# Performance work log

Hardware: AMD Instinct MI355X
Metric: run time of the kernel (lower is better)

Reference implementation:

```python
import jax, jax.numpy as jnp
import numpy as np

HEAD = 16
EPS = 1.1920929e-07  # torch.finfo(float32).eps, used by nn.RMSNorm when eps=None


def _rms(x, g):
    return x * jax.lax.rsqrt(jnp.mean(x * x, axis=-1, keepdims=True) + EPS) * g


def _heads(t):
    b, L, dm = t.shape
    return t.reshape(b, L, HEAD, dm // HEAD).transpose(0, 2, 1, 3)  # b h L d


def setup_inputs() -> dict:
    key = jax.random.key(0)
    ks = jax.random.split(key, 8)
    b, L, dims = 1, 1024, 1024
    s = dims ** -0.5
    x = jax.random.normal(ks[0], (b, L, dims), jnp.float32)
    pt = jax.random.normal(ks[1], (b, L, dims), jnp.float32)
    # additive causal mask (finite large-negative to stay grad-safe)
    mask = jnp.triu(jnp.full((L, L), -1e9, jnp.float32), k=1)
    return {
        "x": x, "pt": pt, "mask": mask,
        "gq": jnp.ones((dims,), jnp.float32),
        "Wq": jax.random.normal(ks[2], (dims, dims), jnp.float32) * s,
        "bq": jnp.zeros((dims,), jnp.float32),
        "gkv": jnp.ones((dims,), jnp.float32),
        "Wkv": jax.random.normal(ks[3], (dims, 2 * dims), jnp.float32) * s,
        "bkv": jnp.zeros((2 * dims,), jnp.float32),
        "gc": jnp.ones((dims,), jnp.float32),
        "Wc": jax.random.normal(ks[4], (dims, dims), jnp.float32) * s,
        "bc": jnp.zeros((dims,), jnp.float32),
        "Wout": jax.random.normal(ks[5], (dims, dims), jnp.float32) * s,
        "bout": jnp.zeros((dims,), jnp.float32),
        "context_window": 16,
    }


def reference(x, pt, mask, gq, Wq, bq, gkv, Wkv, bkv, gc, Wc, bc, Wout, bout, context_window):
    b, L, dims = x.shape
    d = dims // HEAD
    q = _heads(_rms(x, gq) @ Wq + bq)                      # b h L d
    kv = (_rms(x, gkv) @ Wkv + bkv).reshape(b, L, 2, HEAD, d)
    k = kv[:, :, 0].transpose(0, 2, 1, 3)                  # b h L d
    v = kv[:, :, 1].transpose(0, 2, 1, 3)
    c = _heads(_rms(pt, gc) @ Wc + bc)                     # b h L d

    # triplet_scores[i,j] = sum_{t=max(0,min(i,j)-w)}^{min(L,max(i,j)+w)-1} q_i . (k_j * c_t)
    # Vectorize with prefix sums over c: window sum = P[end] - P[start],
    # where end depends only on max(i,j) and start only on min(i,j).
    P = jnp.concatenate([jnp.zeros((b, HEAD, 1, d), x.dtype), jnp.cumsum(c, axis=2)], axis=2)  # b h L+1 d
    idx = jnp.arange(L)
    S = jnp.clip(idx - context_window, 0, L)   # start for min-index
    E = jnp.clip(idx + context_window, 0, L)   # end for max-index
    PE = jnp.take(P, E, axis=2)                # b h L d
    PS = jnp.take(P, S, axis=2)

    U = jnp.einsum('bhid,bhjd->bhij', q, k * PE)        # end from j (i<=j branch)
    V = jnp.einsum('bhid,bhjd->bhij', q * PS, k)        # start from i (i<=j branch)
    U2 = jnp.einsum('bhid,bhjd->bhij', q * PE, k)       # end from i (i>j branch)
    V2 = jnp.einsum('bhid,bhjd->bhij', q, k * PS)       # start from j (i>j branch)
    lower = idx[:, None] <= idx[None, :]
    triplet = jnp.where(lower, U - V, U2 - V2)          # b h L L

    scale = d ** -0.5
    qk = jnp.einsum('bhid,bhjd->bhij', q, k) * scale + triplet + mask[:L, :L]
    attn = jax.nn.softmax(qk, axis=-1)
    wv = jnp.einsum('bhij,bhjd->bhid', attn, v)
    out = wv.transpose(0, 2, 1, 3).reshape(b, L, dims) @ Wout + bout  # dropout p=0.01 is identity at eval
    return out
```

## Files before the change

### kernel.cpp

```cpp
#include <hip/hip_runtime.h>

#define LQ 1024
#define DM 1024


typedef __attribute__((ext_vector_type(8))) short bf16x8;
typedef __attribute__((ext_vector_type(4))) float f32x4;

#define MFMA(a, b, c) __builtin_amdgcn_mfma_f32_16x16x32_bf16((a), (b), (c), 0, 0, 0)

__device__ __forceinline__ unsigned short f2bf(float x) {
    unsigned int u = __float_as_uint(x);
    return (unsigned short)((u + 0x7FFFu + ((u >> 16) & 1u)) >> 16);
}
__device__ __forceinline__ float bf2f(unsigned short h) {
    return __uint_as_float(((unsigned int)h) << 16);
}
__device__ __forceinline__ void gload16(const void* gp, void* lp) {
    __builtin_amdgcn_global_load_lds(
        (const __attribute__((address_space(1))) void*)gp,
        (__attribute__((address_space(3))) void*)lp, 16, 0, 0);
}
__device__ __forceinline__ void store_split4(unsigned short* ph, unsigned short* pl,
                                             float4 v) {
    unsigned short h0 = f2bf(v.x), h1 = f2bf(v.y), h2 = f2bf(v.z), h3 = f2bf(v.w);
    uint2 a;
    a.x = (unsigned)h0 | ((unsigned)h1 << 16);
    a.y = (unsigned)h2 | ((unsigned)h3 << 16);
    *(uint2*)ph = a;
    unsigned short l0 = f2bf(v.x - bf2f(h0)), l1 = f2bf(v.y - bf2f(h1));
    unsigned short l2 = f2bf(v.z - bf2f(h2)), l3 = f2bf(v.w - bf2f(h3));
    uint2 b;
    b.x = (unsigned)l0 | ((unsigned)l1 << 16);
    b.y = (unsigned)l2 | ((unsigned)l3 << 16);
    *(uint2*)pl = b;
}

__global__ __launch_bounds__(256) void rms_kernel(
    const float* __restrict__ x, const float* __restrict__ pt,
    const float* __restrict__ gq, const float* __restrict__ gkv,
    const float* __restrict__ gc,
    unsigned short* __restrict__ xqn_h, unsigned short* __restrict__ xqn_l,
    unsigned short* __restrict__ xkvn_h, unsigned short* __restrict__ xkvn_l,
    unsigned short* __restrict__ ptn_h, unsigned short* __restrict__ ptn_l)
{
    const int row = blockIdx.x;
    const int t = threadIdx.x;
    const bool isx = row < LQ;
    const float* src = isx ? (x + (size_t)row * DM)
                           : (pt + (size_t)(row - LQ) * DM);
    float4 v = ((const float4*)src)[t];
    float ss = v.x*v.x + v.y*v.y + v.z*v.z + v.w*v.w;
    #pragma unroll
    for (int o = 32; o > 0; o >>= 1) ss += __shfl_down(ss, o);
    __shared__ float red[4];
    if ((t & 63) == 0) red[t >> 6] = ss;
    __syncthreads();
    const float r = rsqrtf((red[0] + red[1] + red[2] + red[3]) * (1.0f / DM)
                           + 1.1920929e-07f);
    const size_t base = (size_t)(isx ? row : row - LQ) * DM + t * 4;
    if (isx) {
        float4 g1 = ((const float4*)gq)[t];
        float4 g2 = ((const float4*)gkv)[t];
        float4 y1, y2;
        y1.x = v.x*r*g1.x; y1.y = v.y*r*g1.y; y1.z = v.z*r*g1.z; y1.w = v.w*r*g1.w;
        y2.x = v.x*r*g2.x; y2.y = v.y*r*g2.y; y2.z = v.z*r*g2.z; y2.w = v.w*r*g2.w;
        store_split4(xqn_h + base, xqn_l + base, y1);
        store_split4(xkvn_h + base, xkvn_l + base, y2);
    } else {
        float4 g = ((const float4*)gc)[t];
        float4 y;
        y.x = v.x*r*g.x; y.y = v.y*r*g.y; y.z = v.z*r*g.z; y.w = v.w*r*g.w;
        store_split4(ptn_h + base, ptn_l + base, y);
    }
}

__global__ __launch_bounds__(256) void wsplit_kernel(
    const float* __restrict__ in, unsigned short* __restrict__ oh,
    unsigned short* __restrict__ ol, int K, int N)
{
    __shared__ float T[64 * 65];
    const int t = threadIdx.x;
    const int tx = t & 15, ty = t >> 4;
    const int c0 = blockIdx.x * 64;
    const int r0 = blockIdx.y * 64;
    #pragma unroll
    for (int p = 0; p < 4; ++p) {
        int row = ty + p * 16;
        float4 v = *(const float4*)(in + (size_t)(r0 + row) * N + c0 + tx * 4);
        T[row * 65 + tx * 4 + 0] = v.x;
        T[row * 65 + tx * 4 + 1] = v.y;
        T[row * 65 + tx * 4 + 2] = v.z;
        T[row * 65 + tx * 4 + 3] = v.w;
    }
    __syncthreads();
    #pragma unroll
    for (int p = 0; p < 4; ++p) {
        int n = ty + p * 16;
        float4 w;
        w.x = T[(tx * 4 + 0) * 65 + n];
        w.y = T[(tx * 4 + 1) * 65 + n];
        w.z = T[(tx * 4 + 2) * 65 + n];
        w.w = T[(tx * 4 + 3) * 65 + n];
        size_t o = (size_t)(c0 + n) * K + r0 + tx * 4;
        store_split4(oh + o, ol + o, w);
    }
}

__device__ __forceinline__ void gemm_mfma_128(
    const unsigned short* __restrict__ Ah, const unsigned short* __restrict__ Al,
    const unsigned short* __restrict__ Bh, const unsigned short* __restrict__ Bl,
    const float* __restrict__ bias, float* __restrict__ out, int N, int mt, int nt)
{
    __shared__ unsigned short sA[2][128 * 32];
    __shared__ unsigned short sB[2][128 * 32];
    const int t = threadIdx.x;
    const int lane = t & 63, wid = t >> 6;
    const int wm = wid >> 1, wn = wid & 1;
    const int n16 = lane & 15, quad = lane >> 4;
    f32x4 zero = {0.f, 0.f, 0.f, 0.f};
    f32x4 acc[4][4];
    #pragma unroll
    for (int ms = 0; ms < 4; ++ms)
        #pragma unroll
        for (int ns = 0; ns < 4; ++ns) acc[ms][ns] = zero;

    const int arow = wid * 16 + (lane >> 2);
    const int acol = (lane & 3) * 8;
    for (int kt = 0; kt < 32; ++kt) {
        const int k0 = kt * 32;
        #pragma unroll
        for (int p = 0; p < 2; ++p) {
            const int row = arow + p * 64;
            const size_t ga = (size_t)(mt * 128 + row) * 1024 + k0 + acol;
            const size_t gb = (size_t)(nt * 128 + row) * 1024 + k0 + acol;
            const int lo = p * 2048 + wid * 512;
            gload16(Ah + ga, &sA[0][lo]);
            gload16(Al + ga, &sA[1][lo]);
            gload16(Bh + gb, &sB[0][lo]);
            gload16(Bl + gb, &sB[1][lo]);
        }
        __syncthreads();
        bf16x8 afh[4], afl[4], bfh[4], bfl[4];
        #pragma unroll
        for (int ms = 0; ms < 4; ++ms) {
            int r = wm * 64 + ms * 16 + n16;
            afh[ms] = *(const bf16x8*)&sA[0][r * 32 + quad * 8];
            afl[ms] = *(const bf16x8*)&sA[1][r * 32 + quad * 8];
        }
        #pragma unroll
        for (int ns = 0; ns < 4; ++ns) {
            int r = wn * 64 + ns * 16 + n16;
            bfh[ns] = *(const bf16x8*)&sB[0][r * 32 + quad * 8];
            bfl[ns] = *(const bf16x8*)&sB[1][r * 32 + quad * 8];
        }
        #pragma unroll
        for (int ms = 0; ms < 4; ++ms)
            #pragma unroll
            for (int ns = 0; ns < 4; ++ns) {
                acc[ms][ns] = MFMA(afh[ms], bfh[ns], acc[ms][ns]);
                acc[ms][ns] = MFMA(afh[ms], bfl[ns], acc[ms][ns]);
                acc[ms][ns] = MFMA(afl[ms], bfh[ns], acc[ms][ns]);
            }
        __syncthreads();
    }
    #pragma unroll
    for (int ns = 0; ns < 4; ++ns) {
        const int col = nt * 128 + wn * 64 + ns * 16 + n16;
        const float bv = bias[col];
        #pragma unroll
        for (int ms = 0; ms < 4; ++ms) {
            const int row0 = mt * 128 + wm * 64 + ms * 16 + quad * 4;
            #pragma unroll
            for (int reg = 0; reg < 4; ++reg)
                out[(size_t)(row0 + reg) * N + col] = acc[ms][ns][reg] + bv;
        }
    }
}

__global__ __launch_bounds__(256) void proj_kernel(
    const unsigned short* __restrict__ xqn_h, const unsigned short* __restrict__ xqn_l,
    const unsigned short* __restrict__ xkvn_h, const unsigned short* __restrict__ xkvn_l,
    const unsigned short* __restrict__ ptn_h, const unsigned short* __restrict__ ptn_l,
    const unsigned short* __restrict__ WqT_h, const unsigned short* __restrict__ WqT_l,
    const unsigned short* __restrict__ WkvT_h, const unsigned short* __restrict__ WkvT_l,
    const unsigned short* __restrict__ WcT_h, const unsigned short* __restrict__ WcT_l,
    const float* __restrict__ bq, const float* __restrict__ bkv,
    const float* __restrict__ bc,
    float* __restrict__ Qb, float* __restrict__ KVb, float* __restrict__ Cb)
{
    const int bid = blockIdx.x;
    if (bid < 64) {
        gemm_mfma_128(xqn_h, xqn_l, WqT_h, WqT_l, bq, Qb, 1024, bid >> 3, bid & 7);
    } else if (bid < 192) {
        int b2 = bid - 64;
        gemm_mfma_128(xkvn_h, xkvn_l, WkvT_h, WkvT_l, bkv, KVb, 2048, b2 >> 4, b2 & 15);
    } else {
        int b2 = bid - 192;
        gemm_mfma_128(ptn_h, ptn_l, WcT_h, WcT_l, bc, Cb, 1024, b2 >> 3, b2 & 7);
    }
}

__global__ __launch_bounds__(128) void outgemm_kernel(
    const unsigned short* __restrict__ Ah, const unsigned short* __restrict__ Al,
    const unsigned short* __restrict__ Bh, const unsigned short* __restrict__ Bl,
    const float* __restrict__ bias, float* __restrict__ out)
{
    __shared__ unsigned short sA[2][64 * 32];
    __shared__ unsigned short sB[2][64 * 32];
    const int t = threadIdx.x;
    const int lane = t & 63, w = t >> 6;
    const int n16 = lane & 15, quad = lane >> 4;
    const int mt = blockIdx.y, nt = blockIdx.x;
    f32x4 zero = {0.f, 0.f, 0.f, 0.f};
    f32x4 acc[2][4];
    #pragma unroll
    for (int ms = 0; ms < 2; ++ms)
        #pragma unroll
        for (int ns = 0; ns < 4; ++ns) acc[ms][ns] = zero;

    const int arow = w * 16 + (lane >> 2);
    const int acol = (lane & 3) * 8;
    for (int kt = 0; kt < 32; ++kt) {
        const int k0 = kt * 32;
        #pragma unroll
        for (int p = 0; p < 2; ++p) {
            const int row = arow + p * 32;
            const size_t ga = (size_t)(mt * 64 + row) * 1024 + k0 + acol;
            const size_t gb = (size_t)(nt * 64 + row) * 1024 + k0 + acol;
            const int lo = p * 1024 + w * 512;
            gload16(Ah + ga, &sA[0][lo]);
            gload16(Al + ga, &sA[1][lo]);
            gload16(Bh + gb, &sB[0][lo]);
            gload16(Bl + gb, &sB[1][lo]);
        }
        __syncthreads();
        bf16x8 afh[2], afl[2], bfh[4], bfl[4];
        #pragma unroll
        for (int ms = 0; ms < 2; ++ms) {
            int r = w * 32 + ms * 16 + n16;
            afh[ms] = *(const bf16x8*)&sA[0][r * 32 + quad * 8];
            afl[ms] = *(const bf16x8*)&sA[1][r * 32 + quad * 8];
        }
        #pragma unroll
        for (int ns = 0; ns < 4; ++ns) {
            int r = ns * 16 + n16;
            bfh[ns] = *(const bf16x8*)&sB[0][r * 32 + quad * 8];
            bfl[ns] = *(const bf16x8*)&sB[1][r * 32 + quad * 8];
        }
        #pragma unroll
        for (int ms = 0; ms < 2; ++ms)
            #pragma unroll
            for (int ns = 0; ns < 4; ++ns) {
                acc[ms][ns] = MFMA(afh[ms], bfh[ns], acc[ms][ns]);
                acc[ms][ns] = MFMA(afh[ms], bfl[ns], acc[ms][ns]);
                acc[ms][ns] = MFMA(afl[ms], bfh[ns], acc[ms][ns]);
            }
        __syncthreads();
    }
    #pragma unroll
    for (int ns = 0; ns < 4; ++ns) {
        const int col = nt * 64 + ns * 16 + n16;
        const float bv = bias[col];
        #pragma unroll
        for (int ms = 0; ms < 2; ++ms) {
            const int row0 = mt * 64 + w * 32 + ms * 16 + quad * 4;
            #pragma unroll
            for (int reg = 0; reg < 4; ++reg)
                out[(size_t)(row0 + reg) * 1024 + col] = acc[ms][ns][reg] + bv;
        }
    }
}

__global__ __launch_bounds__(256) void csum_kernel(const float* __restrict__ Cb,
                                                   float* __restrict__ csum)
{
    const int cid = blockIdx.x >> 2;
    const int col = ((blockIdx.x & 3) << 8) + threadIdx.x;
    const float* p = Cb + (size_t)cid * 32 * 1024 + col;
    float s = 0.f;
    #pragma unroll 8
    for (int r = 0; r < 32; ++r) s += p[(size_t)r * 1024];
    csum[cid * 1024 + col] = s;
}

__global__ __launch_bounds__(256) void scanp_kernel(const float* __restrict__ Cb,
                                                    const float* __restrict__ csum,
                                                    float* __restrict__ Pb)
{
    const int cid = blockIdx.x >> 2;
    const int col = ((blockIdx.x & 3) << 8) + threadIdx.x;
    float run = 0.f;
    for (int c = 0; c < cid; ++c) run += csum[c * 1024 + col];
    const float* p = Cb + (size_t)cid * 32 * 1024 + col;
    float* q = Pb + (size_t)cid * 32 * 1024 + col;
    for (int r = 0; r < 32; ++r) {
        q[(size_t)r * 1024] = run;
        run += p[(size_t)r * 1024];
    }
    if (cid == 31) Pb[(size_t)1024 * 1024 + col] = run;
}

__global__ __launch_bounds__(256) void ab_kernel(
    const float* __restrict__ Qb, const float* __restrict__ KVb,
    const float* __restrict__ Pb, const int* __restrict__ cwp,
    unsigned short* __restrict__ Aah, unsigned short* __restrict__ Aal,
    unsigned short* __restrict__ Bah, unsigned short* __restrict__ Bal)
{
    const int gid = blockIdx.x * 256 + threadIdx.x;
    const int i = gid >> 10;
    const int col = gid & 1023;
    const int h = col >> 6, dd = col & 63;
    const int cw = *cwp;
    const int E = min(i + cw, LQ);
    const int S = max(i - cw, 0);
    const float pe = Pb[(size_t)E * 1024 + col];
    const float ps = Pb[(size_t)S * 1024 + col];
    const float q = Qb[gid];
    const float k = KVb[(size_t)i * 2048 + col];
    const float scale = 0.125f;
    const size_t base = ((size_t)(h * 1024 + i)) * 128;
    float a0 = q, a1 = q * pe;
    float b0 = k * (scale - ps), b1 = k;
    unsigned short hv;
    hv = f2bf(a0); Aah[base + dd] = hv;      Aal[base + dd] = f2bf(a0 - bf2f(hv));
    hv = f2bf(a1); Aah[base + 64 + dd] = hv; Aal[base + 64 + dd] = f2bf(a1 - bf2f(hv));
    hv = f2bf(b0); Bah[base + dd] = hv;      Bal[base + dd] = f2bf(b0 - bf2f(hv));
    hv = f2bf(b1); Bah[base + 64 + dd] = hv; Bal[base + 64 + dd] = f2bf(b1 - bf2f(hv));
}

__global__ __launch_bounds__(256) void vprep_kernel(const float* __restrict__ KVb,
                                                    unsigned short* __restrict__ VT)
{
    __shared__ float T[64 * 65];
    const int h = blockIdx.y, j0 = blockIdx.x * 64;
    const int t = threadIdx.x;
    const int tx = t & 15, ty = t >> 4;
    #pragma unroll
    for (int p = 0; p < 4; ++p) {
        int j = ty + p * 16;
        float4 v = *(const float4*)(KVb + (size_t)(j0 + j) * 2048 + 1024 + h * 64 + tx * 4);
        T[j * 65 + tx * 4 + 0] = v.x;
        T[j * 65 + tx * 4 + 1] = v.y;
        T[j * 65 + tx * 4 + 2] = v.z;
        T[j * 65 + tx * 4 + 3] = v.w;
    }
    __syncthreads();
    #pragma unroll
    for (int p = 0; p < 4; ++p) {
        int d = ty + p * 16;
        unsigned short e0 = f2bf(T[(tx * 4 + 0) * 65 + d]);
        unsigned short e1 = f2bf(T[(tx * 4 + 1) * 65 + d]);
        unsigned short e2 = f2bf(T[(tx * 4 + 2) * 65 + d]);
        unsigned short e3 = f2bf(T[(tx * 4 + 3) * 65 + d]);
        uint2 pk;
        pk.x = (unsigned)e0 | ((unsigned)e1 << 16);
        pk.y = (unsigned)e2 | ((unsigned)e3 << 16);
        *(uint2*)(VT + (size_t)(h * 64 + d) * 1024 + j0 + tx * 4) = pk;
    }
}

__global__ __launch_bounds__(128) void attn_kernel(
    const unsigned short* __restrict__ Aah, const unsigned short* __restrict__ Aal,
    const unsigned short* __restrict__ Bah, const unsigned short* __restrict__ Bal,
    const unsigned short* __restrict__ VT,
    unsigned short* __restrict__ wvh, unsigned short* __restrict__ wvl)
{
    __shared__ unsigned short sA[2][32 * 136];
    __shared__ unsigned short sB[2][64 * 136];
    unsigned short* Ps = sB[0];
    unsigned short* Vs = sB[0] + 32 * 136;

    const int t = threadIdx.x;
    const int lane = t & 63, w = t >> 6;
    const int n16 = lane & 15, quad = lane >> 4;
    const int b = blockIdx.x;
    const int g = b >> 8, rr = b & 255;
    const int h = rr & 15;
    const int it = g ? (rr >> 4) : (31 - (rr >> 4));
    const int i0 = it * 32;
    const int njt = (it >> 1) + 1;

    {
        const int r = t >> 2;
        const int cb = (t & 3) * 32;
        const unsigned short* gh = Aah + ((size_t)(h * 1024 + i0 + r)) * 128 + cb;
        const unsigned short* gl = Aal + ((size_t)(h * 1024 + i0 + r)) * 128 + cb;
        #pragma unroll
        for (int u = 0; u < 4; ++u) {
            *(uint4*)&sA[0][r * 136 + cb + u * 8] = *(const uint4*)(gh + u * 8);
            *(uint4*)&sA[1][r * 136 + cb + u * 8] = *(const uint4*)(gl + u * 8);
        }
    }

    f32x4 zero = {0.f, 0.f, 0.f, 0.f};
    f32x4 oacc[4];
    #pragma unroll
    for (int dt = 0; dt < 4; ++dt) oacc[dt] = zero;
    float mrow[4], lrow[4];
    #pragma unroll
    for (int reg = 0; reg < 4; ++reg) { mrow[reg] = -1e30f; lrow[reg] = 0.f; }

    for (int jt64 = 0; jt64 < njt; ++jt64) {
        const int j0 = jt64 * 64;
        __syncthreads();
        {
            const int r = t >> 1;
            const int cb = (t & 1) * 64;
            const unsigned short* gh = Bah + ((size_t)(h * 1024 + j0 + r)) * 128 + cb;
            const unsigned short* gl = Bal + ((size_t)(h * 1024 + j0 + r)) * 128 + cb;
            #pragma unroll
            for (int u = 0; u < 8; ++u) {
                *(uint4*)&sB[0][r * 136 + cb + u * 8] = *(const uint4*)(gh + u * 8);
                *(uint4*)&sB[1][r * 136 + cb + u * 8] = *(const uint4*)(gl + u * 8);
            }
        }
        __syncthreads();

        bf16x8 afh[4], afl[4];
        #pragma unroll
        for (int kc = 0; kc < 4; ++kc) {
            int r = w * 16 + n16;
            afh[kc] = *(const bf16x8*)&sA[0][r * 136 + kc * 32 + quad * 8];
            afl[kc] = *(const bf16x8*)&sA[1][r * 136 + kc * 32 + quad * 8];
        }
        f32x4 s[4];
        #pragma unroll
        for (int jt = 0; jt < 4; ++jt) s[jt] = zero;
        #pragma unroll
        for (int jt = 0; jt < 4; ++jt) {
            #pragma unroll
            for (int kc = 0; kc < 4; ++kc) {
                int r = jt * 16 + n16;
                bf16x8 bh = *(const bf16x8*)&sB[0][r * 136 + kc * 32 + quad * 8];
                bf16x8 bl = *(const bf16x8*)&sB[1][r * 136 + kc * 32 + quad * 8];
                s[jt] = MFMA(afh[kc], bh, s[jt]);
                s[jt] = MFMA(afh[kc], bl, s[jt]);
                s[jt] = MFMA(afl[kc], bh, s[jt]);
            }
        }
        if (jt64 == njt - 1) {
            const int ibase = i0 + w * 16 + quad * 4;
            #pragma unroll
            for (int jt = 0; jt < 4; ++jt) {
                const int j = j0 + jt * 16 + n16;
                #pragma unroll
                for (int reg = 0; reg < 4; ++reg)
                    if (j > ibase + reg) s[jt][reg] = -1e30f;
            }
        }

        float alpha[4];
        #pragma unroll
        for (int reg = 0; reg < 4; ++reg) {
            float mt_ = fmaxf(fmaxf(s[0][reg], s[1][reg]), fmaxf(s[2][reg], s[3][reg]));
            mt_ = fmaxf(mt_, __shfl_xor(mt_, 1));
            mt_ = fmaxf(mt_, __shfl_xor(mt_, 2));
            mt_ = fmaxf(mt_, __shfl_xor(mt_, 4));
            mt_ = fmaxf(mt_, __shfl_xor(mt_, 8));
            const float mn = fmaxf(mrow[reg], mt_);
            alpha[reg] = __expf(mrow[reg] - mn);
            mrow[reg] = mn;
            float rs = 0.f;
            #pragma unroll
            for (int jt = 0; jt < 4; ++jt) {
                float p = __expf(s[jt][reg] - mn);
                s[jt][reg] = p;
                rs += p;
            }
            rs += __shfl_xor(rs, 1); rs += __shfl_xor(rs, 2);
            rs += __shfl_xor(rs, 4); rs += __shfl_xor(rs, 8);
            lrow[reg] = lrow[reg] * alpha[reg] + rs;
        }

        __syncthreads();
        #pragma unroll
        for (int jt = 0; jt < 4; ++jt)
            #pragma unroll
            for (int reg = 0; reg < 4; ++reg)
                Ps[(w * 16 + quad * 4 + reg) * 136 + jt * 16 + n16] = f2bf(s[jt][reg]);
        {
            const int r = t >> 1;
            const int cb = (t & 1) * 32;
            const unsigned short* gv = VT + ((size_t)(h * 64 + r)) * 1024 + j0 + cb;
            #pragma unroll
            for (int u = 0; u < 4; ++u)
                *(uint4*)&Vs[r * 136 + cb + u * 8] = *(const uint4*)(gv + u * 8);
        }
        __syncthreads();

        #pragma unroll
        for (int dt = 0; dt < 4; ++dt)
            #pragma unroll
            for (int reg = 0; reg < 4; ++reg)
                oacc[dt][reg] *= alpha[reg];
        bf16x8 pf[2];
        #pragma unroll
        for (int kc = 0; kc < 2; ++kc)
            pf[kc] = *(const bf16x8*)&Ps[(w * 16 + n16) * 136 + kc * 32 + quad * 8];
        #pragma unroll
        for (int dt = 0; dt < 4; ++dt)
            #pragma unroll
            for (int kc = 0; kc < 2; ++kc) {
                bf16x8 vf = *(const bf16x8*)&Vs[(dt * 16 + n16) * 136 + kc * 32 + quad * 8];
                oacc[dt] = MFMA(pf[kc], vf, oacc[dt]);
            }
    }

    float inv[4];
    #pragma unroll
    for (int reg = 0; reg < 4; ++reg) inv[reg] = 1.0f / lrow[reg];
    #pragma unroll
    for (int dt = 0; dt < 4; ++dt) {
        #pragma unroll
        for (int reg = 0; reg < 4; ++reg) {
            const float v = oacc[dt][reg] * inv[reg];
            const size_t idx = (size_t)(i0 + w * 16 + quad * 4 + reg) * 1024
                             + h * 64 + dt * 16 + n16;
            const unsigned short hv = f2bf(v);
            wvh[idx] = hv;
            wvl[idx] = f2bf(v - bf2f(hv));
        }
    }
}

extern "C" void kernel_launch(void* const* d_in, const int* in_sizes, int n_in,
                              void* d_out, int out_size, void* d_ws, size_t ws_size,
                              hipStream_t stream) {
    (void)in_sizes; (void)n_in; (void)out_size; (void)ws_size;
    const float* x    = (const float*)d_in[0];
    const float* pt   = (const float*)d_in[1];
    const float* gq   = (const float*)d_in[3];
    const float* Wq   = (const float*)d_in[4];
    const float* bq   = (const float*)d_in[5];
    const float* gkv  = (const float*)d_in[6];
    const float* Wkv  = (const float*)d_in[7];
    const float* bkv  = (const float*)d_in[8];
    const float* gc   = (const float*)d_in[9];
    const float* Wc   = (const float*)d_in[10];
    const float* bc   = (const float*)d_in[11];
    const float* Wout = (const float*)d_in[12];
    const float* bout = (const float*)d_in[13];
    const int*   cw   = (const int*)d_in[14];
    float* out = (float*)d_out;

    char* W = (char*)d_ws;
    const size_t MB = 1u << 20;
    #define US(off) ((unsigned short*)(W + (off)))
    #define FP(off) ((float*)(W + (off)))
    unsigned short* xqn_h  = US(0 * MB);
    unsigned short* xqn_l  = US(2 * MB);
    unsigned short* xkvn_h = US(4 * MB);
    unsigned short* xkvn_l = US(6 * MB);
    unsigned short* ptn_h  = US(8 * MB);
    unsigned short* ptn_l  = US(10 * MB);
    unsigned short* WqT_h  = US(12 * MB);
    unsigned short* WqT_l  = US(14 * MB);
    unsigned short* WkvT_h = US(16 * MB);
    unsigned short* WkvT_l = US(20 * MB);
    unsigned short* WcT_h  = US(24 * MB);
    unsigned short* WcT_l  = US(26 * MB);
    unsigned short* WoutT_h = US(28 * MB);
    unsigned short* WoutT_l = US(30 * MB);
    float* Qb   = FP(32 * MB);
    float* KVb  = FP(36 * MB);
    float* Cb   = FP(44 * MB);
    float* Pb   = FP(48 * MB);
    float* csum = FP(53 * MB);
    unsigned short* Aah = US(0 * MB);
    unsigned short* Aal = US(4 * MB);
    unsigned short* Bah = US(8 * MB);
    unsigned short* Bal = US(12 * MB);
    unsigned short* VTb = US(16 * MB);
    unsigned short* wv_h = US(18 * MB);
    unsigned short* wv_l = US(20 * MB);
    #undef US
    #undef FP

    hipLaunchKernelGGL(rms_kernel, dim3(2048), dim3(256), 0, stream,
                       x, pt, gq, gkv, gc, xqn_h, xqn_l, xkvn_h, xkvn_l, ptn_h, ptn_l);
    hipLaunchKernelGGL(wsplit_kernel, dim3(16, 16), dim3(256), 0, stream,
                       Wq, WqT_h, WqT_l, 1024, 1024);
    hipLaunchKernelGGL(wsplit_kernel, dim3(32, 16), dim3(256), 0, stream,
                       Wkv, WkvT_h, WkvT_l, 1024, 2048);
    hipLaunchKernelGGL(wsplit_kernel, dim3(16, 16), dim3(256), 0, stream,
                       Wc, WcT_h, WcT_l, 1024, 1024);
    hipLaunchKernelGGL(wsplit_kernel, dim3(16, 16), dim3(256), 0, stream,
                       Wout, WoutT_h, WoutT_l, 1024, 1024);
    hipLaunchKernelGGL(proj_kernel, dim3(256), dim3(256), 0, stream,
                       xqn_h, xqn_l, xkvn_h, xkvn_l, ptn_h, ptn_l,
                       WqT_h, WqT_l, WkvT_h, WkvT_l, WcT_h, WcT_l,
                       bq, bkv, bc, Qb, KVb, Cb);
    hipLaunchKernelGGL(csum_kernel, dim3(128), dim3(256), 0, stream, Cb, csum);
    hipLaunchKernelGGL(scanp_kernel, dim3(128), dim3(256), 0, stream, Cb, csum, Pb);
    hipLaunchKernelGGL(ab_kernel, dim3(4096), dim3(256), 0, stream,
                       Qb, KVb, Pb, cw, Aah, Aal, Bah, Bal);
    hipLaunchKernelGGL(vprep_kernel, dim3(16, 16), dim3(256), 0, stream, KVb, VTb);
    hipLaunchKernelGGL(attn_kernel, dim3(512), dim3(128), 0, stream,
                       Aah, Aal, Bah, Bal, VTb, wv_h, wv_l);
    hipLaunchKernelGGL(outgemm_kernel, dim3(16, 16), dim3(128), 0, stream,
                       wv_h, wv_l, WoutT_h, WoutT_l, bout, out);
}
```

Measured before the change: 246.2 us.

## Fuse prep kernels, split attention over key halves, merge partials in out-GEMM

Merges the RMS-norm and four weight-split kernels into one launch, and the ab and vprep kernels into another, cutting launch count. The projection GEMM tile now uses 512 threads with a smaller per-wave N sub-tile. Attention becomes split-K: each wave handles 16 query rows for one head and half of the key range, and writes unnormalised partial outputs plus running max and sum. The output GEMM then combines the two partials with log-sum-exp weights while loading its A tile. The aim is more parallelism and better load balance in attention, in exchange for extra fp32 partial traffic and merge work.

New measurement: 276.4 us. 1.12x slower.

```diff
diff --git a/kernel.cpp b/kernel.cpp
--- a/kernel.cpp
+++ b/kernel.cpp
@@ -36,15 +36,14 @@
     *(uint2*)pl = b;
 }
 
-__global__ __launch_bounds__(256) void rms_kernel(
-    const float* __restrict__ x, const float* __restrict__ pt,
+__device__ __forceinline__ void rms_body(
+    int row, const float* __restrict__ x, const float* __restrict__ pt,
     const float* __restrict__ gq, const float* __restrict__ gkv,
     const float* __restrict__ gc,
-    unsigned short* __restrict__ xqn_h, unsigned short* __restrict__ xqn_l,
-    unsigned short* __restrict__ xkvn_h, unsigned short* __restrict__ xkvn_l,
-    unsigned short* __restrict__ ptn_h, unsigned short* __restrict__ ptn_l)
-{
-    const int row = blockIdx.x;
+    unsigned short* xqn_h, unsigned short* xqn_l,
+    unsigned short* xkvn_h, unsigned short* xkvn_l,
+    unsigned short* ptn_h, unsigned short* ptn_l)
+{
     const int t = threadIdx.x;
     const bool isx = row < LQ;
     const float* src = isx ? (x + (size_t)row * DM)
@@ -75,15 +74,14 @@
     }
 }
 
-__global__ __launch_bounds__(256) void wsplit_kernel(
-    const float* __restrict__ in, unsigned short* __restrict__ oh,
-    unsigned short* __restrict__ ol, int K, int N)
+__device__ __forceinline__ void wsplit_body(
+    const float* __restrict__ in, unsigned short* oh, unsigned short* ol,
+    int K, int N, int bx, int by)
 {
     __shared__ float T[64 * 65];
     const int t = threadIdx.x;
     const int tx = t & 15, ty = t >> 4;
-    const int c0 = blockIdx.x * 64;
-    const int r0 = blockIdx.y * 64;
+    const int c0 = bx * 64, r0 = by * 64;
     #pragma unroll
     for (int p = 0; p < 4; ++p) {
         int row = ty + p * 16;
@@ -107,66 +105,89 @@
     }
 }
 
-__device__ __forceinline__ void gemm_mfma_128(
+__global__ __launch_bounds__(256) void prep_kernel(
+    const float* __restrict__ x, const float* __restrict__ pt,
+    const float* __restrict__ gq, const float* __restrict__ gkv,
+    const float* __restrict__ gc,
+    const float* __restrict__ Wq, const float* __restrict__ Wkv,
+    const float* __restrict__ Wc, const float* __restrict__ Wout,
+    unsigned short* xqn_h, unsigned short* xqn_l,
+    unsigned short* xkvn_h, unsigned short* xkvn_l,
+    unsigned short* ptn_h, unsigned short* ptn_l,
+    unsigned short* WqT_h, unsigned short* WqT_l,
+    unsigned short* WkvT_h, unsigned short* WkvT_l,
+    unsigned short* WcT_h, unsigned short* WcT_l,
+    unsigned short* WoT_h, unsigned short* WoT_l)
+{
+    const int b = blockIdx.x;
+    if (b < 2048) {
+        rms_body(b, x, pt, gq, gkv, gc, xqn_h, xqn_l, xkvn_h, xkvn_l, ptn_h, ptn_l);
+    } else if (b < 2304) {
+        int s = b - 2048; wsplit_body(Wq, WqT_h, WqT_l, 1024, 1024, s & 15, s >> 4);
+    } else if (b < 2816) {
+        int s = b - 2304; wsplit_body(Wkv, WkvT_h, WkvT_l, 1024, 2048, s & 31, s >> 5);
+    } else if (b < 3072) {
+        int s = b - 2816; wsplit_body(Wc, WcT_h, WcT_l, 1024, 1024, s & 15, s >> 4);
+    } else {
+        int s = b - 3072; wsplit_body(Wout, WoT_h, WoT_l, 1024, 1024, s & 15, s >> 4);
+    }
+}
+
+__device__ __forceinline__ void gemm3p(
     const unsigned short* __restrict__ Ah, const unsigned short* __restrict__ Al,
     const unsigned short* __restrict__ Bh, const unsigned short* __restrict__ Bl,
     const float* __restrict__ bias, float* __restrict__ out, int N, int mt, int nt)
 {
-    __shared__ unsigned short sA[2][128 * 32];
-    __shared__ unsigned short sB[2][128 * 32];
+    __shared__ unsigned short sAh[128 * 32], sAl[128 * 32];
+    __shared__ unsigned short sBh[128 * 32], sBl[128 * 32];
     const int t = threadIdx.x;
-    const int lane = t & 63, wid = t >> 6;
-    const int wm = wid >> 1, wn = wid & 1;
+    const int lane = t & 63, w = t >> 6;
+    const int wm = w >> 2, wn = w & 3;
     const int n16 = lane & 15, quad = lane >> 4;
+    const int srow = lane >> 2, scol = (lane & 3) * 8;
     f32x4 zero = {0.f, 0.f, 0.f, 0.f};
-    f32x4 acc[4][4];
+    f32x4 acc[4][2];
     #pragma unroll
     for (int ms = 0; ms < 4; ++ms)
         #pragma unroll
-        for (int ns = 0; ns < 4; ++ns) acc[ms][ns] = zero;
-
-    const int arow = wid * 16 + (lane >> 2);
-    const int acol = (lane & 3) * 8;
+        for (int ns = 0; ns < 2; ++ns) acc[ms][ns] = zero;
+
     for (int kt = 0; kt < 32; ++kt) {
         const int k0 = kt * 32;
-        #pragma unroll
-        for (int p = 0; p < 2; ++p) {
-            const int row = arow + p * 64;
-            const size_t ga = (size_t)(mt * 128 + row) * 1024 + k0 + acol;
-            const size_t gb = (size_t)(nt * 128 + row) * 1024 + k0 + acol;
-            const int lo = p * 2048 + wid * 512;
-            gload16(Ah + ga, &sA[0][lo]);
-            gload16(Al + ga, &sA[1][lo]);
-            gload16(Bh + gb, &sB[0][lo]);
-            gload16(Bl + gb, &sB[1][lo]);
-        }
+        const size_t ga = (size_t)(mt * 128 + w * 16 + srow) * 1024 + k0 + scol;
+        const size_t gb = (size_t)(nt * 128 + w * 16 + srow) * 1024 + k0 + scol;
+        const int lb = w * 512;
         __syncthreads();
-        bf16x8 afh[4], afl[4], bfh[4], bfl[4];
+        gload16(Ah + ga, sAh + lb);
+        gload16(Al + ga, sAl + lb);
+        gload16(Bh + gb, sBh + lb);
+        gload16(Bl + gb, sBl + lb);
+        __syncthreads();
+        bf16x8 afh[4], afl[4], bfh[2], bfl[2];
         #pragma unroll
         for (int ms = 0; ms < 4; ++ms) {
             int r = wm * 64 + ms * 16 + n16;
-            afh[ms] = *(const bf16x8*)&sA[0][r * 32 + quad * 8];
-            afl[ms] = *(const bf16x8*)&sA[1][r * 32 + quad * 8];
-        }
-        #pragma unroll
-        for (int ns = 0; ns < 4; ++ns) {
-            int r = wn * 64 + ns * 16 + n16;
-            bfh[ns] = *(const bf16x8*)&sB[0][r * 32 + quad * 8];
-            bfl[ns] = *(const bf16x8*)&sB[1][r * 32 + quad * 8];
+            afh[ms] = *(const bf16x8*)&sAh[r * 32 + quad * 8];
+            afl[ms] = *(const bf16x8*)&sAl[r * 32 + quad * 8];
+        }
+        #pragma unroll
+        for (int ns = 0; ns < 2; ++ns) {
+            int r = wn * 32 + ns * 16 + n16;
+            bfh[ns] = *(const bf16x8*)&sBh[r * 32 + quad * 8];
+            bfl[ns] = *(const bf16x8*)&sBl[r * 32 + quad * 8];
         }
         #pragma unroll
         for (int ms = 0; ms < 4; ++ms)
             #pragma unroll
-            for (int ns = 0; ns < 4; ++ns) {
+            for (int ns = 0; ns < 2; ++ns) {
                 acc[ms][ns] = MFMA(afh[ms], bfh[ns], acc[ms][ns]);
                 acc[ms][ns] = MFMA(afh[ms], bfl[ns], acc[ms][ns]);
                 acc[ms][ns] = MFMA(afl[ms], bfh[ns], acc[ms][ns]);
             }
-        __syncthreads();
-    }
-    #pragma unroll
-    for (int ns = 0; ns < 4; ++ns) {
-        const int col = nt * 128 + wn * 64 + ns * 16 + n16;
+    }
+    #pragma unroll
+    for (int ns = 0; ns < 2; ++ns) {
+        const int col = nt * 128 + wn * 32 + ns * 16 + n16;
         const float bv = bias[col];
         #pragma unroll
         for (int ms = 0; ms < 4; ++ms) {
@@ -178,7 +199,7 @@
     }
 }
 
-__global__ __launch_bounds__(256) void proj_kernel(
+__global__ __launch_bounds__(512) void proj_kernel(
     const unsigned short* __restrict__ xqn_h, const unsigned short* __restrict__ xqn_l,
     const unsigned short* __restrict__ xkvn_h, const unsigned short* __restrict__ xkvn_l,
     const unsigned short* __restrict__ ptn_h, const unsigned short* __restrict__ ptn_l,
@@ -191,84 +212,13 @@
 {
     const int bid = blockIdx.x;
     if (bid < 64) {
-        gemm_mfma_128(xqn_h, xqn_l, WqT_h, WqT_l, bq, Qb, 1024, bid >> 3, bid & 7);
+        gemm3p(xqn_h, xqn_l, WqT_h, WqT_l, bq, Qb, 1024, bid >> 3, bid & 7);
     } else if (bid < 192) {
         int b2 = bid - 64;
-        gemm_mfma_128(xkvn_h, xkvn_l, WkvT_h, WkvT_l, bkv, KVb, 2048, b2 >> 4, b2 & 15);
+        gemm3p(xkvn_h, xkvn_l, WkvT_h, WkvT_l, bkv, KVb, 2048, b2 >> 4, b2 & 15);
     } else {
         int b2 = bid - 192;
-        gemm_mfma_128(ptn_h, ptn_l, WcT_h, WcT_l, bc, Cb, 1024, b2 >> 3, b2 & 7);
-    }
-}
-
-__global__ __launch_bounds__(128) void outgemm_kernel(
-    const unsigned short* __restrict__ Ah, const unsigned short* __restrict__ Al,
-    const unsigned short* __restrict__ Bh, const unsigned short* __restrict__ Bl,
-    const float* __restrict__ bias, float* __restrict__ out)
-{
-    __shared__ unsigned short sA[2][64 * 32];
-    __shared__ unsigned short sB[2][64 * 32];
-    const int t = threadIdx.x;
-    const int lane = t & 63, w = t >> 6;
-    const int n16 = lane & 15, quad = lane >> 4;
-    const int mt = blockIdx.y, nt = blockIdx.x;
-    f32x4 zero = {0.f, 0.f, 0.f, 0.f};
-    f32x4 acc[2][4];
-    #pragma unroll
-    for (int ms = 0; ms < 2; ++ms)
-        #pragma unroll
-        for (int ns = 0; ns < 4; ++ns) acc[ms][ns] = zero;
-
-    const int arow = w * 16 + (lane >> 2);
-    const int acol = (lane & 3) * 8;
-    for (int kt = 0; kt < 32; ++kt) {
-        const int k0 = kt * 32;
-        #pragma unroll
-        for (int p = 0; p < 2; ++p) {
-            const int row = arow + p * 32;
-            const size_t ga = (size_t)(mt * 64 + row) * 1024 + k0 + acol;
-            const size_t gb = (size_t)(nt * 64 + row) * 1024 + k0 + acol;
-            const int lo = p * 1024 + w * 512;
-            gload16(Ah + ga, &sA[0][lo]);
-            gload16(Al + ga, &sA[1][lo]);
-            gload16(Bh + gb, &sB[0][lo]);
-            gload16(Bl + gb, &sB[1][lo]);
-        }
-        __syncthreads();
-        bf16x8 afh[2], afl[2], bfh[4], bfl[4];
-        #pragma unroll
-        for (int ms = 0; ms < 2; ++ms) {
-            int r = w * 32 + ms * 16 + n16;
-            afh[ms] = *(const bf16x8*)&sA[0][r * 32 + quad * 8];
-            afl[ms] = *(const bf16x8*)&sA[1][r * 32 + quad * 8];
-        }
-        #pragma unroll
-        for (int ns = 0; ns < 4; ++ns) {
-            int r = ns * 16 + n16;
-            bfh[ns] = *(const bf16x8*)&sB[0][r * 32 + quad * 8];
-            bfl[ns] = *(const bf16x8*)&sB[1][r * 32 + quad * 8];
-        }
-        #pragma unroll
-        for (int ms = 0; ms < 2; ++ms)
-            #pragma unroll
-            for (int ns = 0; ns < 4; ++ns) {
-                acc[ms][ns] = MFMA(afh[ms], bfh[ns], acc[ms][ns]);
-                acc[ms][ns] = MFMA(afh[ms], bfl[ns], acc[ms][ns]);
-                acc[ms][ns] = MFMA(afl[ms], bfh[ns], acc[ms][ns]);
-            }
-        __syncthreads();
-    }
-    #pragma unroll
-    for (int ns = 0; ns < 4; ++ns) {
-        const int col = nt * 64 + ns * 16 + n16;
-        const float bv = bias[col];
-        #pragma unroll
-        for (int ms = 0; ms < 2; ++ms) {
-            const int row0 = mt * 64 + w * 32 + ms * 16 + quad * 4;
-            #pragma unroll
-            for (int reg = 0; reg < 4; ++reg)
-                out[(size_t)(row0 + reg) * 1024 + col] = acc[ms][ns][reg] + bv;
-        }
+        gemm3p(ptn_h, ptn_l, WcT_h, WcT_l, bc, Cb, 1024, b2 >> 3, b2 & 7);
     }
 }
 
@@ -301,95 +251,92 @@
     if (cid == 31) Pb[(size_t)1024 * 1024 + col] = run;
 }
 
-__global__ __launch_bounds__(256) void ab_kernel(
+__global__ __launch_bounds__(256) void abv_kernel(
     const float* __restrict__ Qb, const float* __restrict__ KVb,
     const float* __restrict__ Pb, const int* __restrict__ cwp,
     unsigned short* __restrict__ Aah, unsigned short* __restrict__ Aal,
-    unsigned short* __restrict__ Bah, unsigned short* __restrict__ Bal)
-{
-    const int gid = blockIdx.x * 256 + threadIdx.x;
-    const int i = gid >> 10;
-    const int col = gid & 1023;
-    const int h = col >> 6, dd = col & 63;
-    const int cw = *cwp;
-    const int E = min(i + cw, LQ);
-    const int S = max(i - cw, 0);
-    const float pe = Pb[(size_t)E * 1024 + col];
-    const float ps = Pb[(size_t)S * 1024 + col];
-    const float q = Qb[gid];
-    const float k = KVb[(size_t)i * 2048 + col];
-    const float scale = 0.125f;
-    const size_t base = ((size_t)(h * 1024 + i)) * 128;
-    float a0 = q, a1 = q * pe;
-    float b0 = k * (scale - ps), b1 = k;
-    unsigned short hv;
-    hv = f2bf(a0); Aah[base + dd] = hv;      Aal[base + dd] = f2bf(a0 - bf2f(hv));
-    hv = f2bf(a1); Aah[base + 64 + dd] = hv; Aal[base + 64 + dd] = f2bf(a1 - bf2f(hv));
-    hv = f2bf(b0); Bah[base + dd] = hv;      Bal[base + dd] = f2bf(b0 - bf2f(hv));
-    hv = f2bf(b1); Bah[base + 64 + dd] = hv; Bal[base + 64 + dd] = f2bf(b1 - bf2f(hv));
-}
-
-__global__ __launch_bounds__(256) void vprep_kernel(const float* __restrict__ KVb,
-                                                    unsigned short* __restrict__ VT)
-{
-    __shared__ float T[64 * 65];
-    const int h = blockIdx.y, j0 = blockIdx.x * 64;
-    const int t = threadIdx.x;
-    const int tx = t & 15, ty = t >> 4;
-    #pragma unroll
-    for (int p = 0; p < 4; ++p) {
-        int j = ty + p * 16;
-        float4 v = *(const float4*)(KVb + (size_t)(j0 + j) * 2048 + 1024 + h * 64 + tx * 4);
-        T[j * 65 + tx * 4 + 0] = v.x;
-        T[j * 65 + tx * 4 + 1] = v.y;
-        T[j * 65 + tx * 4 + 2] = v.z;
-        T[j * 65 + tx * 4 + 3] = v.w;
-    }
-    __syncthreads();
-    #pragma unroll
-    for (int p = 0; p < 4; ++p) {
-        int d = ty + p * 16;
-        unsigned short e0 = f2bf(T[(tx * 4 + 0) * 65 + d]);
-        unsigned short e1 = f2bf(T[(tx * 4 + 1) * 65 + d]);
-        unsigned short e2 = f2bf(T[(tx * 4 + 2) * 65 + d]);
-        unsigned short e3 = f2bf(T[(tx * 4 + 3) * 65 + d]);
-        uint2 pk;
-        pk.x = (unsigned)e0 | ((unsigned)e1 << 16);
-        pk.y = (unsigned)e2 | ((unsigned)e3 << 16);
-        *(uint2*)(VT + (size_t)(h * 64 + d) * 1024 + j0 + tx * 4) = pk;
-    }
-}
-
-__global__ __launch_bounds__(128) void attn_kernel(
+    unsigned short* __restrict__ Bah, unsigned short* __restrict__ Bal,
+    unsigned short* __restrict__ VT)
+{
+    const int b = blockIdx.x;
+    if (b < 4096) {
+        const int gid = b * 256 + threadIdx.x;
+        const int i = gid >> 10;
+        const int col = gid & 1023;
+        const int h = col >> 6, dd = col & 63;
+        const int cw = *cwp;
+        const int E = min(i + cw, LQ);
+        const int S = max(i - cw, 0);
+        const float pe = Pb[(size_t)E * 1024 + col];
+        const float ps = Pb[(size_t)S * 1024 + col];
+        const float q = Qb[gid];
+        const float k = KVb[(size_t)i * 2048 + col];
+        const float scale = 0.125f;
+        const size_t base = ((size_t)(h * 1024 + i)) * 128;
+        float a0 = q, a1 = q * pe;
+        float b0 = k * (scale - ps), b1 = k;
+        unsigned short hv;
+        hv = f2bf(a0); Aah[base + dd] = hv;      Aal[base + dd] = f2bf(a0 - bf2f(hv));
+        hv = f2bf(a1); Aah[base + 64 + dd] = hv; Aal[base + 64 + dd] = f2bf(a1 - bf2f(hv));
+        hv = f2bf(b0); Bah[base + dd] = hv;      Bal[base + dd] = f2bf(b0 - bf2f(hv));
+        hv = f2bf(b1); Bah[base + 64 + dd] = hv; Bal[base + 64 + dd] = f2bf(b1 - bf2f(hv));
+    } else {
+        const int s = b - 4096;
+        const int h = s >> 4, j0 = (s & 15) * 64;
+        __shared__ float T[64 * 65];
+        const int t = threadIdx.x;
+        const int tx = t & 15, ty = t >> 4;
+        #pragma unroll
+        for (int p = 0; p < 4; ++p) {
+            int j = ty + p * 16;
+            float4 v = *(const float4*)(KVb + (size_t)(j0 + j) * 2048 + 1024 + h * 64 + tx * 4);
+            T[j * 65 + tx * 4 + 0] = v.x;
+            T[j * 65 + tx * 4 + 1] = v.y;
+            T[j * 65 + tx * 4 + 2] = v.z;
+            T[j * 65 + tx * 4 + 3] = v.w;
+        }
+        __syncthreads();
+        #pragma unroll
+        for (int p = 0; p < 4; ++p) {
+            int d = ty + p * 16;
+            unsigned short e0 = f2bf(T[(tx * 4 + 0) * 65 + d]);
+            unsigned short e1 = f2bf(T[(tx * 4 + 1) * 65 + d]);
+            unsigned short e2 = f2bf(T[(tx * 4 + 2) * 65 + d]);
+            unsigned short e3 = f2bf(T[(tx * 4 + 3) * 65 + d]);
+            uint2 pk;
+            pk.x = (unsigned)e0 | ((unsigned)e1 << 16);
+            pk.y = (unsigned)e2 | ((unsigned)e3 << 16);
+            *(uint2*)(VT + (size_t)(h * 64 + d) * 1024 + j0 + tx * 4) = pk;
+        }
+    }
+}
+
+__global__ __launch_bounds__(256) void attn_kernel(
     const unsigned short* __restrict__ Aah, const unsigned short* __restrict__ Aal,
     const unsigned short* __restrict__ Bah, const unsigned short* __restrict__ Bal,
     const unsigned short* __restrict__ VT,
-    unsigned short* __restrict__ wvh, unsigned short* __restrict__ wvl)
-{
-    __shared__ unsigned short sA[2][32 * 136];
-    __shared__ unsigned short sB[2][64 * 136];
-    unsigned short* Ps = sB[0];
-    unsigned short* Vs = sB[0] + 32 * 136;
-
+    float* __restrict__ Op, float* __restrict__ Mp, float* __restrict__ Lp)
+{
+    __shared__ unsigned short PsAll[4][16 * 68];
     const int t = threadIdx.x;
-    const int lane = t & 63, w = t >> 6;
+    const int lane = t & 63, wid = t >> 6;
+    unsigned short* Ps = PsAll[wid];
+    const int raw = blockIdx.x * 4 + wid;
+    const int g = raw >> 5;
+    const int it16 = (g & 1) ? (g >> 1) : (63 - (g >> 1));
+    const int sub = raw & 31;
+    const int h = sub >> 1, half = sub & 1;
+    const int i0 = it16 * 16;
+    const int njt = (i0 >> 6) + 1;
     const int n16 = lane & 15, quad = lane >> 4;
-    const int b = blockIdx.x;
-    const int g = b >> 8, rr = b & 255;
-    const int h = rr & 15;
-    const int it = g ? (rr >> 4) : (31 - (rr >> 4));
-    const int i0 = it * 32;
-    const int njt = (it >> 1) + 1;
-
+
+    bf16x8 afh[4], afl[4];
     {
-        const int r = t >> 2;
-        const int cb = (t & 3) * 32;
-        const unsigned short* gh = Aah + ((size_t)(h * 1024 + i0 + r)) * 128 + cb;
-        const unsigned short* gl = Aal + ((size_t)(h * 1024 + i0 + r)) * 128 + cb;
-        #pragma unroll
-        for (int u = 0; u < 4; ++u) {
-            *(uint4*)&sA[0][r * 136 + cb + u * 8] = *(const uint4*)(gh + u * 8);
-            *(uint4*)&sA[1][r * 136 + cb + u * 8] = *(const uint4*)(gl + u * 8);
+        const size_t ar = ((size_t)(h * 1024 + i0 + n16)) * 128 + quad * 8;
+        #pragma unroll
+        for (int kc = 0; kc < 4; ++kc) {
+            afh[kc] = *(const bf16x8*)(Aah + ar + kc * 32);
+            afl[kc] = *(const bf16x8*)(Aal + ar + kc * 32);
         }
     }
 
@@ -401,52 +348,31 @@
     #pragma unroll
     for (int reg = 0; reg < 4; ++reg) { mrow[reg] = -1e30f; lrow[reg] = 0.f; }
 
-    for (int jt64 = 0; jt64 < njt; ++jt64) {
-        const int j0 = jt64 * 64;
-        __syncthreads();
-        {
-            const int r = t >> 1;
-            const int cb = (t & 1) * 64;
-            const unsigned short* gh = Bah + ((size_t)(h * 1024 + j0 + r)) * 128 + cb;
-            const unsigned short* gl = Bal + ((size_t)(h * 1024 + j0 + r)) * 128 + cb;
-            #pragma unroll
-            for (int u = 0; u < 8; ++u) {
-                *(uint4*)&sB[0][r * 136 + cb + u * 8] = *(const uint4*)(gh + u * 8);
-                *(uint4*)&sB[1][r * 136 + cb + u * 8] = *(const uint4*)(gl + u * 8);
+    for (int jt = half; jt < njt; jt += 2) {
+        const int j0 = jt * 64;
+        f32x4 s[4];
+        #pragma unroll
+        for (int jj = 0; jj < 4; ++jj) s[jj] = zero;
+        #pragma unroll
+        for (int jj = 0; jj < 4; ++jj) {
+            const size_t br = ((size_t)(h * 1024 + j0 + jj * 16 + n16)) * 128 + quad * 8;
+            #pragma unroll
+            for (int kc = 0; kc < 4; ++kc) {
+                bf16x8 bh = *(const bf16x8*)(Bah + br + kc * 32);
+                bf16x8 bl = *(const bf16x8*)(Bal + br + kc * 32);
+                s[jj] = MFMA(afh[kc], bh, s[jj]);
+                s[jj] = MFMA(afh[kc], bl, s[jj]);
+                s[jj] = MFMA(afl[kc], bh, s[jj]);
             }
         }
-        __syncthreads();
-
-        bf16x8 afh[4], afl[4];
-        #pragma unroll
-        for (int kc = 0; kc < 4; ++kc) {
-            int r = w * 16 + n16;
-            afh[kc] = *(const bf16x8*)&sA[0][r * 136 + kc * 32 + quad * 8];
-            afl[kc] = *(const bf16x8*)&sA[1][r * 136 + kc * 32 + quad * 8];
-        }
-        f32x4 s[4];
-        #pragma unroll
-        for (int jt = 0; jt < 4; ++jt) s[jt] = zero;
-        #pragma unroll
-        for (int jt = 0; jt < 4; ++jt) {
-            #pragma unroll
-            for (int kc = 0; kc < 4; ++kc) {
-                int r = jt * 16 + n16;
-                bf16x8 bh = *(const bf16x8*)&sB[0][r * 136 + kc * 32 + quad * 8];
-                bf16x8 bl = *(const bf16x8*)&sB[1][r * 136 + kc * 32 + quad * 8];
-                s[jt] = MFMA(afh[kc], bh, s[jt]);
-                s[jt] = MFMA(afh[kc], bl, s[jt]);
-                s[jt] = MFMA(afl[kc], bh, s[jt]);
-            }
-        }
-        if (jt64 == njt - 1) {
-            const int ibase = i0 + w * 16 + quad * 4;
-            #pragma unroll
-            for (int jt = 0; jt < 4; ++jt) {
-                const int j = j0 + jt * 16 + n16;
+        if (jt == njt - 1) {
+            const int ibase = i0 + quad * 4;
+            #pragma unroll
+            for (int jj = 0; jj < 4; ++jj) {
+                const int j = j0 + jj * 16 + n16;
                 #pragma unroll
                 for (int reg = 0; reg < 4; ++reg)
-                    if (j > ibase + reg) s[jt][reg] = -1e30f;
+                    if (j > ibase + reg) s[jj][reg] = -1e30f;
             }
         }
 
@@ -463,9 +389,9 @@
             mrow[reg] = mn;
             float rs = 0.f;
             #pragma unroll
-            for (int jt = 0; jt < 4; ++jt) {
-                float p = __expf(s[jt][reg] - mn);
-                s[jt][reg] = p;
+            for (int jj = 0; jj < 4; ++jj) {
+                float p = __expf(s[jj][reg] - mn);
+                s[jj][reg] = p;
                 rs += p;
             }
             rs += __shfl_xor(rs, 1); rs += __shfl_xor(rs, 2);
@@ -473,53 +399,136 @@
             lrow[reg] = lrow[reg] * alpha[reg] + rs;
         }
 
+        __builtin_amdgcn_s_waitcnt(0xC07F);
+        #pragma unroll
+        for (int jj = 0; jj < 4; ++jj)
+            #pragma unroll
+            for (int reg = 0; reg < 4; ++reg)
+                Ps[(quad * 4 + reg) * 68 + jj * 16 + n16] = f2bf(s[jj][reg]);
+        __builtin_amdgcn_s_waitcnt(0xC07F);
+        bf16x8 pf0 = *(const bf16x8*)&Ps[n16 * 68 + quad * 8];
+        bf16x8 pf1 = *(const bf16x8*)&Ps[n16 * 68 + 32 + quad * 8];
+
+        #pragma unroll
+        for (int dt = 0; dt < 4; ++dt) {
+            #pragma unroll
+            for (int reg = 0; reg < 4; ++reg) oacc[dt][reg] *= alpha[reg];
+            const size_t vr = ((size_t)(h * 64 + dt * 16 + n16)) * 1024 + j0 + quad * 8;
+            bf16x8 vf0 = *(const bf16x8*)(VT + vr);
+            bf16x8 vf1 = *(const bf16x8*)(VT + vr + 32);
+            oacc[dt] = MFMA(pf0, vf0, oacc[dt]);
+            oacc[dt] = MFMA(pf1, vf1, oacc[dt]);
+        }
+    }
+
+    const int tid = (h * 64 + it16) * 2 + half;
+    #pragma unroll
+    for (int dt = 0; dt < 4; ++dt)
+        #pragma unroll
+        for (int reg = 0; reg < 4; ++reg)
+            Op[(size_t)tid * 1024 + (quad * 4 + reg) * 64 + dt * 16 + n16] = oacc[dt][reg];
+    if (n16 == 0) {
+        #pragma unroll
+        for (int reg = 0; reg < 4; ++reg) {
+            Mp[tid * 16 + quad * 4 + reg] = mrow[reg];
+            Lp[tid * 16 + quad * 4 + reg] = lrow[reg];
+        }
+    }
+}
+
+__global__ __launch_bounds__(128) void outgemm_kernel(
+    const float* __restrict__ Op, const float* __restrict__ Mp,
+    const float* __restrict__ Lp,
+    const unsigned short* __restrict__ WoT_h, const unsigned short* __restrict__ WoT_l,
+    const float* __restrict__ bout, float* __restrict__ out)
+{
+    __shared__ float cc[16 * 64 * 2];
+    __shared__ unsigned short sAh[64 * 32], sAl[64 * 32];
+    __shared__ unsigned short sBh[32 * 32], sBl[32 * 32];
+    const int t = threadIdx.x;
+    const int lane = t & 63, w = t >> 6;
+    const int n16 = lane & 15, quad = lane >> 4;
+    const int mt = blockIdx.x >> 5, nt = blockIdx.x & 31;
+
+    for (int p = t; p < 1024; p += 128) {
+        const int hh = p >> 6, row = p & 63;
+        const int i = mt * 64 + row, i16 = i >> 4, r = i & 15;
+        const int t0 = (hh * 64 + i16) * 2;
+        const float m1 = Mp[t0 * 16 + r], m2 = Mp[(t0 + 1) * 16 + r];
+        const float l1 = Lp[t0 * 16 + r], l2 = Lp[(t0 + 1) * 16 + r];
+        const float M = fmaxf(m1, m2);
+        const float e1 = __expf(m1 - M), e2 = __expf(m2 - M);
+        const float Ltot = e1 * l1 + e2 * l2;
+        cc[p * 2 + 0] = e1 / Ltot;
+        cc[p * 2 + 1] = e2 / Ltot;
+    }
+
+    f32x4 zero = {0.f, 0.f, 0.f, 0.f};
+    f32x4 acc[2][2];
+    #pragma unroll
+    for (int ms = 0; ms < 2; ++ms)
+        #pragma unroll
+        for (int ns = 0; ns < 2; ++ns) acc[ms][ns] = zero;
+
+    const int arow = t >> 1, aseg = (t & 1) * 16;
+    for (int kt = 0; kt < 32; ++kt) {
+        const int hh = kt >> 1, dbase = (kt & 1) * 32;
         __syncthreads();
-        #pragma unroll
-        for (int jt = 0; jt < 4; ++jt)
+        {
+            const size_t gb = (size_t)(nt * 32 + w * 16 + (lane >> 2)) * 1024
+                            + kt * 32 + (lane & 3) * 8;
+            gload16(WoT_h + gb, sBh + w * 512);
+            gload16(WoT_l + gb, sBl + w * 512);
+        }
+        {
+            const int i = mt * 64 + arow, i16 = i >> 4, r = i & 15;
+            const float c1 = cc[(hh * 64 + arow) * 2 + 0];
+            const float c2 = cc[(hh * 64 + arow) * 2 + 1];
+            const size_t b0 = ((size_t)((hh * 64 + i16) * 2)) * 1024 + r * 64 + dbase + aseg;
+            #pragma unroll
+            for (int u = 0; u < 4; ++u) {
+                float4 o1 = *(const float4*)(Op + b0 + u * 4);
+                float4 o2 = *(const float4*)(Op + b0 + 1024 + u * 4);
+                float4 v;
+                v.x = c1 * o1.x + c2 * o2.x; v.y = c1 * o1.y + c2 * o2.y;
+                v.z = c1 * o1.z + c2 * o2.z; v.w = c1 * o1.w + c2 * o2.w;
+                store_split4(&sAh[arow * 32 + aseg + u * 4],
+                             &sAl[arow * 32 + aseg + u * 4], v);
+            }
+        }
+        __syncthreads();
+        bf16x8 ah[2], al[2], bh[2], bl[2];
+        #pragma unroll
+        for (int ms = 0; ms < 2; ++ms) {
+            int r = w * 32 + ms * 16 + n16;
+            ah[ms] = *(const bf16x8*)&sAh[r * 32 + quad * 8];
+            al[ms] = *(const bf16x8*)&sAl[r * 32 + quad * 8];
+        }
+        #pragma unroll
+        for (int ns = 0; ns < 2; ++ns) {
+            int r = ns * 16 + n16;
+            bh[ns] = *(const bf16x8*)&sBh[r * 32 + quad * 8];
+            bl[ns] = *(const bf16x8*)&sBl[r * 32 + quad * 8];
+        }
+        #pragma unroll
+        for (int ms = 0; ms < 2; ++ms)
+            #pragma unroll
+            for (int ns = 0; ns < 2; ++ns) {
+                acc[ms][ns] = MFMA(ah[ms], bh[ns], acc[ms][ns]);
+                acc[ms][ns] = MFMA(ah[ms], bl[ns], acc[ms][ns]);
+                acc[ms][ns] = MFMA(al[ms], bh[ns], acc[ms][ns]);
+            }
+    }
+    #pragma unroll
+    for (int ns = 0; ns < 2; ++ns) {
+        const int col = nt * 32 + ns * 16 + n16;
+        const float bv = bout[col];
+        #pragma unroll
+        for (int ms = 0; ms < 2; ++ms) {
+            const int row0 = mt * 64 + w * 32 + ms * 16 + quad * 4;
             #pragma unroll
             for (int reg = 0; reg < 4; ++reg)
-                Ps[(w * 16 + quad * 4 + reg) * 136 + jt * 16 + n16] = f2bf(s[jt][reg]);
-        {
-            const int r = t >> 1;
-            const int cb = (t & 1) * 32;
-            const unsigned short* gv = VT + ((size_t)(h * 64 + r)) * 1024 + j0 + cb;
-            #pragma unroll
-            for (int u = 0; u < 4; ++u)
-                *(uint4*)&Vs[r * 136 + cb + u * 8] = *(const uint4*)(gv + u * 8);
-        }
-        __syncthreads();
-
-        #pragma unroll
-        for (int dt = 0; dt < 4; ++dt)
-            #pragma unroll
-            for (int reg = 0; reg < 4; ++reg)
-                oacc[dt][reg] *= alpha[reg];
-        bf16x8 pf[2];
-        #pragma unroll
-        for (int kc = 0; kc < 2; ++kc)
-            pf[kc] = *(const bf16x8*)&Ps[(w * 16 + n16) * 136 + kc * 32 + quad * 8];
-        #pragma unroll
-        for (int dt = 0; dt < 4; ++dt)
-            #pragma unroll
-            for (int kc = 0; kc < 2; ++kc) {
-                bf16x8 vf = *(const bf16x8*)&Vs[(dt * 16 + n16) * 136 + kc * 32 + quad * 8];
-                oacc[dt] = MFMA(pf[kc], vf, oacc[dt]);
-            }
-    }
-
-    float inv[4];
-    #pragma unroll
-    for (int reg = 0; reg < 4; ++reg) inv[reg] = 1.0f / lrow[reg];
-    #pragma unroll
-    for (int dt = 0; dt < 4; ++dt) {
-        #pragma unroll
-        for (int reg = 0; reg < 4; ++reg) {
-            const float v = oacc[dt][reg] * inv[reg];
-            const size_t idx = (size_t)(i0 + w * 16 + quad * 4 + reg) * 1024
-                             + h * 64 + dt * 16 + n16;
-            const unsigned short hv = f2bf(v);
-            wvh[idx] = hv;
-            wvl[idx] = f2bf(v - bf2f(hv));
+                out[(size_t)(row0 + reg) * 1024 + col] = acc[ms][ns][reg] + bv;
         }
     }
 }
@@ -546,8 +555,8 @@
 
     char* W = (char*)d_ws;
     const size_t MB = 1u << 20;
-    #define US(off) ((unsigned short*)(W + (off)))
-    #define FP(off) ((float*)(W + (off)))
+    #define US(off) ((unsigned short*)(W + (size_t)(off)))
+    #define FP(off) ((float*)(W + (size_t)(off)))
     unsigned short* xqn_h  = US(0 * MB);
     unsigned short* xqn_l  = US(2 * MB);
     unsigned short* xkvn_h = US(4 * MB);
@@ -560,44 +569,38 @@
     unsigned short* WkvT_l = US(20 * MB);
     unsigned short* WcT_h  = US(24 * MB);
     unsigned short* WcT_l  = US(26 * MB);
-    unsigned short* WoutT_h = US(28 * MB);
-    unsigned short* WoutT_l = US(30 * MB);
+    unsigned short* WoT_h  = US(28 * MB);
+    unsigned short* WoT_l  = US(30 * MB);
     float* Qb   = FP(32 * MB);
     float* KVb  = FP(36 * MB);
     float* Cb   = FP(44 * MB);
     float* Pb   = FP(48 * MB);
-    float* csum = FP(53 * MB);
+    float* csum = FP(52 * MB + 256 * 1024);
     unsigned short* Aah = US(0 * MB);
     unsigned short* Aal = US(4 * MB);
     unsigned short* Bah = US(8 * MB);
     unsigned short* Bal = US(12 * MB);
     unsigned short* VTb = US(16 * MB);
-    unsigned short* wv_h = US(18 * MB);
-    unsigned short* wv_l = US(20 * MB);
+    float* Op = FP(18 * MB);
+    float* Mp = FP(26 * MB);
+    float* Lp = FP(26 * MB + 512 * 1024);
     #undef US
     #undef FP
 
-    hipLaunchKernelGGL(rms_kernel, dim3(2048), dim3(256), 0, stream,
-                       x, pt, gq, gkv, gc, xqn_h, xqn_l, xkvn_h, xkvn_l, ptn_h, ptn_l);
-    hipLaunchKernelGGL(wsplit_kernel, dim3(16, 16), dim3(256), 0, stream,
-                       Wq, WqT_h, WqT_l, 1024, 1024);
-    hipLaunchKernelGGL(wsplit_kernel, dim3(32, 16), dim3(256), 0, stream,
-                       Wkv, WkvT_h, WkvT_l, 1024, 2048);
-    hipLaunchKernelGGL(wsplit_kernel, dim3(16, 16), dim3(256), 0, stream,
-                       Wc, WcT_h, WcT_l, 1024, 1024);
-    hipLaunchKernelGGL(wsplit_kernel, dim3(16, 16), dim3(256), 0, stream,
-                       Wout, WoutT_h, WoutT_l, 1024, 1024);
-    hipLaunchKernelGGL(proj_kernel, dim3(256), dim3(256), 0, stream,
+    hipLaunchKernelGGL(prep_kernel, dim3(3328), dim3(256), 0, stream,
+                       x, pt, gq, gkv, gc, Wq, Wkv, Wc, Wout,
+                       xqn_h, xqn_l, xkvn_h, xkvn_l, ptn_h, ptn_l,
+                       WqT_h, WqT_l, WkvT_h, WkvT_l, WcT_h, WcT_l, WoT_h, WoT_l);
+    hipLaunchKernelGGL(proj_kernel, dim3(256), dim3(512), 0, stream,
                        xqn_h, xqn_l, xkvn_h, xkvn_l, ptn_h, ptn_l,
                        WqT_h, WqT_l, WkvT_h, WkvT_l, WcT_h, WcT_l,
                        bq, bkv, bc, Qb, KVb, Cb);
     hipLaunchKernelGGL(csum_kernel, dim3(128), dim3(256), 0, stream, Cb, csum);
     hipLaunchKernelGGL(scanp_kernel, dim3(128), dim3(256), 0, stream, Cb, csum, Pb);
-    hipLaunchKernelGGL(ab_kernel, dim3(4096), dim3(256), 0, stream,
-                       Qb, KVb, Pb, cw, Aah, Aal, Bah, Bal);
-    hipLaunchKernelGGL(vprep_kernel, dim3(16, 16), dim3(256), 0, stream, KVb, VTb);
-    hipLaunchKernelGGL(attn_kernel, dim3(512), dim3(128), 0, stream,
-                       Aah, Aal, Bah, Bal, VTb, wv_h, wv_l);
-    hipLaunchKernelGGL(outgemm_kernel, dim3(16, 16), dim3(128), 0, stream,
-                       wv_h, wv_l, WoutT_h, WoutT_l, bout, out);
-}
+    hipLaunchKernelGGL(abv_kernel, dim3(4352), dim3(256), 0, stream,
+                       Qb, KVb, Pb, cw, Aah, Aal, Bah, Bal, VTb);
+    hipLaunchKernelGGL(attn_kernel, dim3(512), dim3(256), 0, stream,
+                       Aah, Aal, Bah, Bal, VTb, Op, Mp, Lp);
+    hipLaunchKernelGGL(outgemm_kernel, dim3(512), dim3(128), 0, stream,
+                       Op, Mp, Lp, WoT_h, WoT_l, bout, out);
+}
```
